# Kernel optimization log

Hardware: AMD Instinct MI355X
Metric: run time of the kernel (lower is better)

The kernel has to match this reference:

```python
import jax, jax.numpy as jnp
import numpy as np

BINS = np.array([1, 2, 3, 4, 8, 16, 32, 64], dtype=np.int32)


def setup_inputs() -> dict:
    N, G, F, H, K = 1024, 620, 20, 150, 128
    D_in = 3 * G + F  # 1880
    key = jax.random.key(0)
    ks = jax.random.split(key, 10)
    g = jax.random.normal(ks[0], (N, G), dtype=jnp.float32)
    si = jax.random.normal(ks[1], (N,), dtype=jnp.float32)
    i1 = jnp.sort(jax.random.randint(ks[2], (N,), 0, 8192)).astype(jnp.int32)
    i2 = jnp.sort(jax.random.randint(ks[3], (N,), 0, 8192)).astype(jnp.int32)
    dist_emb = jax.random.normal(ks[4], (9, F), dtype=jnp.float32) * 0.02
    W1 = jax.random.normal(ks[5], (D_in, H), dtype=jnp.float32) * (1.0 / np.sqrt(D_in))
    b1 = jnp.zeros((H,), jnp.float32)
    W2 = jax.random.normal(ks[6], (H, H), dtype=jnp.float32) * (1.0 / np.sqrt(H))
    b2 = jnp.zeros((H,), jnp.float32)
    W3 = jax.random.normal(ks[7], (H, 1), dtype=jnp.float32) * (1.0 / np.sqrt(H))
    b3 = jnp.zeros((1,), jnp.float32)
    return {"g": g, "si": si, "i1": i1, "i2": i2, "dist_emb": dist_emb,
            "W1": W1, "b1": b1, "W2": W2, "b2": b2, "W3": W3, "b3": b3, "K": K}


def reference(g, si, i1, i2, dist_emb, W1, b1, W2, b2, W3, b3, K):
    # Dropout is inference-disabled; epsilon dummy antecedent appended as last column.
    N, G = g.shape
    # span n's antecedents are spans [max(0, n-K), n); lay out as [N, K] window
    j_idx = jnp.arange(N)[:, None] - K + jnp.arange(K)[None, :]  # [N, K]
    valid = j_idx >= 0
    j = jnp.clip(j_idx, 0, N - 1)
    g_j = g[j]                      # [N, K, G] ragged gather (masked dense)
    g_i = g[:, None, :]             # [N, 1, G]
    # distance feature: bin(i.i2 - j.i1) with idx = #bins <= d
    d = i2[:, None] - i1[j]         # [N, K]
    bin_idx = jnp.searchsorted(jnp.asarray(BINS), d, side='right')
    de = dist_emb[bin_idx]          # [N, K, F]
    pairs = jnp.concatenate(
        [jnp.broadcast_to(g_i, (N, K, G)), g_j, g_i * g_j, de], axis=-1)  # [N, K, 3G+F]
    h = jax.nn.relu(jnp.einsum('nkd,dh->nkh', pairs, W1) + b1)
    h = jax.nn.relu(jnp.einsum('nkh,hm->nkm', h, W2) + b2)
    s = (jnp.einsum('nkh,ho->nko', h, W3) + b3)[..., 0]  # [N, K]
    sij = si[:, None] + si[j] + s
    sij = jnp.where(valid, sij, 0.0)
    eps = jnp.zeros((N, 1), sij.dtype)  # epsilon dummy score
    return jnp.concatenate([sij, eps], axis=-1)  # [N, K+1]
```

## Files before the change

### kernel.cpp

```cpp
#include <hip/hip_runtime.h>
#include <hip/hip_bf16.h>
#include <stdint.h>

typedef __attribute__((ext_vector_type(8))) short short8;
typedef __attribute__((ext_vector_type(4))) float float4_t;

#define N_PTS 1024
#define G_DIM 620
#define G_PAD 640
#define F_DIM 20
#define H_DIM 150
#define H_PAD 160
#define K_WIN 128
#define OUT_C (K_WIN + 1)

__device__ __forceinline__ float bf2f(short u) {
  union { unsigned int i; float f; } x;
  x.i = ((unsigned int)(unsigned short)u) << 16;
  return x.f;
}
__device__ __forceinline__ short f2bf(float f) {
  union { float f; unsigned int i; } x; x.f = f;
  unsigned int u = x.i;
  u += 0x7FFFu + ((u >> 16) & 1u);
  return (short)(u >> 16);
}
__device__ __forceinline__ short f2bf_hw(float f) {
  __hip_bfloat16 h = __float2bfloat16(f);
  union { __hip_bfloat16 h; short s; } u; u.h = h;
  return u.s;
}
__device__ __forceinline__ void gload_lds16(const void* g, void* l) {
  __builtin_amdgcn_global_load_lds(
      (const __attribute__((address_space(1))) unsigned int*)g,
      (__attribute__((address_space(3))) unsigned int*)l, 16, 0, 0);
}

__global__ void prep_pack(const float* __restrict__ g, const float* __restrict__ W1,
                          const float* __restrict__ W2, const float* __restrict__ dist_emb,
                          short* __restrict__ g_bf, short* __restrict__ W1cT,
                          short* __restrict__ W1abT, short* __restrict__ W2T,
                          float* __restrict__ deW) {
  __shared__ float lds[32 * 165];
  const int bx = blockIdx.x, tid = threadIdx.x;
  if (bx < 256) {
    const int n0 = bx * 4;
    for (int c = tid; c < 320; c += 256) {
      int r = c / 80, cc = c - r * 80;
      int n = n0 + r, d0 = cc * 8;
      short8 o;
      if (d0 + 8 <= G_DIM) {
        const float* src = g + n * G_DIM + d0;
        #pragma unroll
        for (int e = 0; e < 8; ++e) o[e] = f2bf(src[e]);
      } else {
        #pragma unroll
        for (int e = 0; e < 8; ++e) {
          int d = d0 + e;
          o[e] = (d < G_DIM) ? f2bf(g[n * G_DIM + d]) : (short)0;
        }
      }
      *(short8*)(g_bf + n * G_PAD + d0) = o;
    }
  } else if (bx < 316) {
    const int tb = bx - 256;
    const int third = tb / 20, dt = tb - third * 20;
    const int d0 = dt * 32;
    for (int c = tid; c < 1280; c += 256) {
      int dr = c / 40, ch4 = c - dr * 40;
      int dd = d0 + dr;
      int w1r = third * G_DIM + dd;
      #pragma unroll
      for (int e = 0; e < 4; ++e) {
        int h = ch4 * 4 + e;
        lds[dr * 165 + h] = (dd < G_DIM && h < H_DIM) ? W1[w1r * H_DIM + h] : 0.f;
      }
    }
    __syncthreads();
    short* outp = (third == 2) ? W1cT : (W1abT + third * H_PAD * G_PAD);
    for (int c = tid; c < 640; c += 256) {
      int h = c >> 2, ch = c & 3;
      short8 o;
      #pragma unroll
      for (int e = 0; e < 8; ++e) o[e] = f2bf(lds[(ch * 8 + e) * 165 + h]);
      *(short8*)(outp + h * G_PAD + d0 + ch * 8) = o;
    }
  } else if (bx < 320) {
    const int base = (bx - 316) * 6400;
    for (int c = tid; c < 6400; c += 256) {
      int q = base + c;
      int m = q / H_PAD, k = q - m * H_PAD;
      W2T[q] = (m < H_DIM && k < H_DIM) ? f2bf(W2[k * H_DIM + m]) : (short)0;
    }
  } else {
    for (int c = tid; c < 9 * H_PAD; c += 256) {
      int b = c / H_PAD, h = c - b * H_PAD;
      float acc = 0.f;
      if (h < H_DIM)
        for (int f = 0; f < F_DIM; ++f)
          acc += dist_emb[b * F_DIM + f] * W1[(3 * G_DIM + f) * H_DIM + h];
      deW[c] = acc;
    }
  }
}

__global__ __launch_bounds__(256) void prep_uv_mfma(
    const short* __restrict__ g_bf, const short* __restrict__ W1abT,
    const short* __restrict__ W1cT, const float* __restrict__ b1,
    float* __restrict__ U, float* __restrict__ V, short* __restrict__ W1cF) {
  if (blockIdx.x >= 32) {
    const int s = (blockIdx.x - 32) + 5 * blockIdx.y;
    const int tid = threadIdx.x;
    #pragma unroll
    for (int it = 0; it < 5; ++it) {
      int slot = tid + 256 * it;
      int lc = slot >> 6, lane = slot & 63;
      int ks = lc / 10, wn = (lc / 5) & 1, nt = lc % 5;
      int lo4 = lane & 15, hi2 = lane >> 4;
      short8 v = *(const short8*)(W1cT + (wn * 80 + nt * 16 + lo4) * G_PAD +
                                  s * 64 + ks * 32 + hi2 * 8);
      *(short8*)(W1cF + (s * 20 + lc) * 512 + lane * 8) = v;
    }
    return;
  }
  __shared__ __align__(16) char sA[32 * 128];
  __shared__ __align__(16) char sB[160 * 128];
  const int m0 = blockIdx.x * 32;
  const int yb = blockIdx.y * H_PAD;
  const int tid = threadIdx.x, lane = tid & 63, wid = tid >> 6;
  const int wm = wid >> 1, wn = wid & 1;
  const int lo4 = lane & 15, hi2 = lane >> 4;
  const int l8 = lane >> 3, c8 = lane & 7;
  const int xe = (c8 ^ (l8 & 7)) * 8;

  const float4_t fz = {0.f, 0.f, 0.f, 0.f};
  float4_t acc[5];
  #pragma unroll
  for (int b = 0; b < 5; ++b) acc[b] = fz;

  for (int step = 0; step < 10; ++step) {
    const int d0 = step * 64;
    {
      int row = wid * 8 + l8;
      gload_lds16(g_bf + (m0 + row) * G_PAD + d0 + xe, sA + (wid * 8) * 128);
    }
    #pragma unroll
    for (int cc = 0; cc < 5; ++cc) {
      int row = wid * 8 + cc * 32 + l8;
      gload_lds16(W1abT + (yb + row) * G_PAD + d0 + xe, sB + (wid * 8 + cc * 32) * 128);
    }
    __syncthreads();
    #pragma unroll
    for (int ks = 0; ks < 2; ++ks) {
      const int kb = ks * 64 + 16 * hi2;
      short8 af, bq[5];
      {
        int row = wm * 16 + lo4;
        af = *((const short8*)(sA + row * 128 + (kb ^ ((row & 7) << 4))));
      }
      #pragma unroll
      for (int nt = 0; nt < 5; ++nt) {
        int row = wn * 80 + nt * 16 + lo4;
        bq[nt] = *((const short8*)(sB + row * 128 + (kb ^ ((row & 7) << 4))));
      }
      #pragma unroll
      for (int nt = 0; nt < 5; ++nt)
        acc[nt] = __builtin_amdgcn_mfma_f32_16x16x32_bf16(af, bq[nt], acc[nt], 0, 0, 0);
    }
    __syncthreads();
  }

  const bool isU = (blockIdx.y == 0);
  float* O = isU ? U : V;
  #pragma unroll
  for (int r = 0; r < 4; ++r) {
    int m = m0 + wm * 16 + hi2 * 4 + r;
    #pragma unroll
    for (int nt = 0; nt < 5; ++nt) {
      int h = wn * 80 + nt * 16 + lo4;
      float v = acc[nt][r];
      if (h < H_DIM) { if (isU) v += b1[h]; } else { v = 0.f; }
      O[m * H_PAD + h] = v;
    }
  }
}

__global__ __launch_bounds__(256, 2) void pair_main(
    const short* __restrict__ g_bf, const short* __restrict__ W1cF,
    const short* __restrict__ W2T, const float* __restrict__ U,
    const float* __restrict__ V, const float* __restrict__ deW,
    const float* __restrict__ si, const int* __restrict__ i1,
    const int* __restrict__ i2, const float* __restrict__ W3,
    const float* __restrict__ b2, const float* __restrict__ b3,
    float* __restrict__ out) {
  __shared__ __align__(16) char smem[49152];
  __shared__ __align__(16) short gi_s[G_PAD];
  __shared__ float sj_s[K_WIN];
  __shared__ unsigned char bin_su[K_WIN];
  __shared__ float s_buf[2][K_WIN];

  char* const P0 = smem;
  char* const P1 = smem + 16384;
  char* const Hb = smem;

  const int bid = blockIdx.x;
  const int i = ((bid & 7) << 7) | (bid >> 3);
  const int tid = threadIdx.x;
  const int lane = tid & 63;
  const int wid = tid >> 6;
  const int wm = wid >> 1, wn = wid & 1;
  const int lo4 = lane & 15, hi2 = lane >> 4;
  const int tc8 = tid & 7;

  if (tid < G_PAD / 8)
    ((short8*)gi_s)[tid] = ((const short8*)(g_bf + i * G_PAD))[tid];
  if (tid < K_WIN) {
    int jr = i - K_WIN + tid, jc = jr < 0 ? 0 : jr;
    int d = i2[i] - i1[jc];
    bin_su[tid] = (unsigned char)((d >= 1) + (d >= 2) + (d >= 3) + (d >= 4) +
                                  (d >= 8) + (d >= 16) + (d >= 32) + (d >= 64));
    sj_s[tid] = si[jc];
  }
  __syncthreads();

  const short8* const bfp = (const short8*)W1cF;

  auto loadBq = [&](int s, short8 (&bq)[2][5]) {
    #pragma unroll
    for (int ks = 0; ks < 2; ++ks)
      #pragma unroll
      for (int nt = 0; nt < 5; ++nt)
        bq[ks][nt] = bfp[(s * 20 + (ks * 2 + wn) * 5 + nt) * 64 + lane];
  };
  auto loadA = [&](int s, short8 (&gjv)[4], short8& gvv) {
    const int d0 = s * 64;
    gvv = *((const short8*)(gi_s + d0 + tc8 * 8));
    #pragma unroll
    for (int cc = 0; cc < 4; ++cc) {
      int c = tid + 256 * cc, row = c >> 3;
      int jr = i - K_WIN + row, jc = jr < 0 ? 0 : jr;
      gjv[cc] = *((const short8*)(g_bf + jc * G_PAD + d0 + tc8 * 8));
    }
  };
  auto writeP = [&](char* P, const short8 (&gjv)[4], const short8& gvv) {
    #pragma unroll
    for (int cc = 0; cc < 4; ++cc) {
      int c = tid + 256 * cc, row = c >> 3;
      short8 p;
      #pragma unroll
      for (int e = 0; e < 8; ++e) p[e] = f2bf_hw(bf2f(gjv[cc][e]) * bf2f(gvv[e]));
      int byte = row * 128 + ((tc8 * 16) ^ ((row & 7) << 4));
      *((short8*)(P + byte)) = p;
    }
  };

  const float4_t fz = {0.f, 0.f, 0.f, 0.f};
  float4_t acc[4][5];
  #pragma unroll
  for (int a = 0; a < 4; ++a)
    #pragma unroll
    for (int b = 0; b < 5; ++b) acc[a][b] = fz;

  auto mfma_step = [&](const char* Pc, const short8 (&bq)[2][5]) {
    __builtin_amdgcn_s_setprio(1);
    #pragma unroll
    for (int ks = 0; ks < 2; ++ks) {
      const int kb = ks * 64 + 16 * hi2;
      short8 af[4];
      #pragma unroll
      for (int mt = 0; mt < 4; ++mt) {
        int row = wm * 64 + mt * 16 + lo4;
        af[mt] = *((const short8*)(Pc + row * 128 + (kb ^ ((row & 7) << 4))));
      }
      #pragma unroll
      for (int mt = 0; mt < 4; ++mt)
        #pragma unroll
        for (int nt = 0; nt < 5; ++nt)
          acc[mt][nt] = __builtin_amdgcn_mfma_f32_16x16x32_bf16(af[mt], bq[ks][nt], acc[mt][nt], 0, 0, 0);
    }
    __builtin_amdgcn_s_setprio(0);
  };

  short8 gjv[4], gvv;
  short8 bqE[2][5], bqO[2][5];
  loadA(0, gjv, gvv);
  loadBq(0, bqE);
  writeP(P0, gjv, gvv);

  #pragma unroll
  for (int ss = 0; ss < 5; ++ss) {
    const int s0 = 2 * ss;
    __syncthreads();
    loadA(s0 + 1, gjv, gvv);
    loadBq(s0 + 1, bqO);
    mfma_step(P0, bqE);
    writeP(P1, gjv, gvv);
    __syncthreads();
    if (ss < 4) {
      loadA(s0 + 2, gjv, gvv);
      loadBq(s0 + 2, bqE);
      mfma_step(P1, bqO);
      writeP(P0, gjv, gvv);
    } else {
      mfma_step(P1, bqO);
    }
  }
  __syncthreads();

  float uih[5];
  #pragma unroll
  for (int nt = 0; nt < 5; ++nt) uih[nt] = U[i * H_PAD + wn * 80 + nt * 16 + lo4];
  #pragma unroll
  for (int mt = 0; mt < 4; ++mt) {
    #pragma unroll
    for (int r = 0; r < 4; ++r) {
      int m = wm * 64 + mt * 16 + hi2 * 4 + r;
      int jr = i - K_WIN + m, jc = jr < 0 ? 0 : jr;
      const float* Vj = V + jc * H_PAD;
      const float* De = deW + bin_su[m] * H_PAD;
      #pragma unroll
      for (int nt = 0; nt < 5; ++nt) {
        int h = wn * 80 + nt * 16 + lo4;
        float val = acc[mt][nt][r] + uih[nt] + Vj[h] + De[h];
        val = (h < H_DIM) ? fmaxf(val, 0.f) : 0.f;
        int tile = h >> 6, hc = h & 63;
        int byte = tile * 16384 + m * 128 + ((hc * 2) ^ ((m & 7) << 4));
        *((short*)(Hb + byte)) = f2bf_hw(val);
      }
    }
  }
  {
    short8 z = {0, 0, 0, 0, 0, 0, 0, 0};
    for (int c = tid; c < 512; c += 256) {
      int row = c >> 2, cb = c & 3;
      int byte = 2 * 16384 + row * 128 + ((64 + cb * 16) ^ ((row & 7) << 4));
      *((short8*)(Hb + byte)) = z;
    }
  }
  __syncthreads();

  float4_t acc2[4][5];
  #pragma unroll
  for (int a = 0; a < 4; ++a)
    #pragma unroll
    for (int b = 0; b < 5; ++b) acc2[a][b] = fz;

  short8 bql[2][5];
  #pragma unroll
  for (int nt = 0; nt < 5; ++nt) {
    int row = wn * 80 + nt * 16 + lo4;
    bql[0][nt] = *(const short8*)(W2T + row * H_PAD + hi2 * 8);
  }
  #pragma unroll
  for (int ks = 0; ks < 5; ++ks) {
    const int cur = ks & 1;
    if (ks < 4) {
      #pragma unroll
      for (int nt = 0; nt < 5; ++nt) {
        int row = wn * 80 + nt * 16 + lo4;
        bql[cur ^ 1][nt] = *(const short8*)(W2T + row * H_PAD + (ks + 1) * 32 + hi2 * 8);
      }
    }
    short8 af[4];
    #pragma unroll
    for (int mt = 0; mt < 4; ++mt) {
      int row = wm * 64 + mt * 16 + lo4;
      int kb = (ks & 1) * 64 + hi2 * 16;
      af[mt] = *((const short8*)(Hb + (ks >> 1) * 16384 + row * 128 + (kb ^ ((row & 7) << 4))));
    }
    __builtin_amdgcn_s_setprio(1);
    #pragma unroll
    for (int mt = 0; mt < 4; ++mt)
      #pragma unroll
      for (int nt = 0; nt < 5; ++nt)
        acc2[mt][nt] = __builtin_amdgcn_mfma_f32_16x16x32_bf16(af[mt], bql[cur][nt], acc2[mt][nt], 0, 0, 0);
    __builtin_amdgcn_s_setprio(0);
  }

  float sp[4][4];
  #pragma unroll
  for (int mt = 0; mt < 4; ++mt)
    #pragma unroll
    for (int r = 0; r < 4; ++r) sp[mt][r] = 0.f;

  #pragma unroll
  for (int nt = 0; nt < 5; ++nt) {
    int h = wn * 80 + nt * 16 + lo4;
    float w3 = (h < H_DIM) ? W3[h] : 0.f;
    float bb = (h < H_DIM) ? b2[h] : 0.f;
    #pragma unroll
    for (int mt = 0; mt < 4; ++mt)
      #pragma unroll
      for (int r = 0; r < 4; ++r) {
        float hv = fmaxf(acc2[mt][nt][r] + bb, 0.f);
        sp[mt][r] += hv * w3;
      }
  }
  #pragma unroll
  for (int mt = 0; mt < 4; ++mt)
    #pragma unroll
    for (int r = 0; r < 4; ++r) {
      float v = sp[mt][r];
      v += __shfl_xor(v, 1);
      v += __shfl_xor(v, 2);
      v += __shfl_xor(v, 4);
      v += __shfl_xor(v, 8);
      sp[mt][r] = v;
    }
  if (lo4 == 0) {
    #pragma unroll
    for (int mt = 0; mt < 4; ++mt)
      #pragma unroll
      for (int r = 0; r < 4; ++r) {
        int m = wm * 64 + mt * 16 + hi2 * 4 + r;
        s_buf[wn][m] = sp[mt][r];
      }
  }
  __syncthreads();

  if (tid < K_WIN) {
    int m = tid;
    int jr = i - K_WIN + m;
    float sij = si[i] + sj_s[m] + s_buf[0][m] + s_buf[1][m] + b3[0];
    out[i * OUT_C + m] = (jr >= 0) ? sij : 0.f;
  }
  if (tid == K_WIN) out[i * OUT_C + K_WIN] = 0.f;
}

extern "C" void kernel_launch(void* const* d_in, const int* in_sizes, int n_in,
                              void* d_out, int out_size, void* d_ws, size_t ws_size,
                              hipStream_t stream) {
  const float* g  = (const float*)d_in[0];
  const float* si = (const float*)d_in[1];
  const int*   i1 = (const int*)d_in[2];
  const int*   i2 = (const int*)d_in[3];
  const float* de = (const float*)d_in[4];
  const float* W1 = (const float*)d_in[5];
  const float* b1 = (const float*)d_in[6];
  const float* W2 = (const float*)d_in[7];
  const float* b2 = (const float*)d_in[8];
  const float* W3 = (const float*)d_in[9];
  const float* b3 = (const float*)d_in[10];
  float* out = (float*)d_out;

  char* ws = (char*)d_ws;
  short* g_bf  = (short*)(ws);
  short* W1cT  = (short*)(ws + 1310720);
  short* W1abT = (short*)(ws + 1515520);
  short* W2T   = (short*)(ws + 1925120);
  float* U     = (float*)(ws + 1976320);
  float* V     = (float*)(ws + 2631680);
  float* deW   = (float*)(ws + 3287040);
  short* W1cF  = (short*)(ws + 3292800);

  prep_pack<<<321, 256, 0, stream>>>(g, W1, W2, de, g_bf, W1cT, W1abT, W2T, deW);
  prep_uv_mfma<<<dim3(37, 2), 256, 0, stream>>>(g_bf, W1abT, W1cT, b1, U, V, W1cF);
  pair_main<<<N_PTS, 256, 0, stream>>>(g_bf, W1cF, W2T, U, V, deW,
                                       si, i1, i2, W3, b2, b3, out);
}
```

Baseline: 72.35 us.

## Stage g_j window via direct global-to-LDS loads and fuse gi product into fragments

Stops loading g_j into registers, multiplying by g_i and writing the product to LDS. Instead the raw g_j window is copied straight from global memory into swizzled LDS with async global-to-LDS loads, and the g_i*g_j product is formed per fragment right before the MFMAs. This frees registers and removes a register round-trip and VALU work from the staging path. Occupancy is also raised by setting launch bounds to 3 blocks per CU. The cost is that both column-half waves now compute the same products, and the tighter register budget may cause spills.

```diff
diff --git a/kernel.cpp b/kernel.cpp
--- a/kernel.cpp
+++ b/kernel.cpp
@@ -185,7 +185,7 @@
   }
 }
 
-__global__ __launch_bounds__(256, 2) void pair_main(
+__global__ __launch_bounds__(256, 3) void pair_main(
     const short* __restrict__ g_bf, const short* __restrict__ W1cF,
     const short* __restrict__ W2T, const float* __restrict__ U,
     const float* __restrict__ V, const float* __restrict__ deW,
@@ -199,8 +199,8 @@
   __shared__ unsigned char bin_su[K_WIN];
   __shared__ float s_buf[2][K_WIN];
 
-  char* const P0 = smem;
-  char* const P1 = smem + 16384;
+  char* const Wn0 = smem;
+  char* const Wn1 = smem + 16384;
   char* const Hb = smem;
 
   const int bid = blockIdx.x;
@@ -210,7 +210,8 @@
   const int wid = tid >> 6;
   const int wm = wid >> 1, wn = wid & 1;
   const int lo4 = lane & 15, hi2 = lane >> 4;
-  const int tc8 = tid & 7;
+  const int l8 = lane >> 3, c8 = lane & 7;
+  const int xe = (c8 ^ (l8 & 7)) * 8;
 
   if (tid < G_PAD / 8)
     ((short8*)gi_s)[tid] = ((const short8*)(g_bf + i * G_PAD))[tid];
@@ -232,25 +233,13 @@
       for (int nt = 0; nt < 5; ++nt)
         bq[ks][nt] = bfp[(s * 20 + (ks * 2 + wn) * 5 + nt) * 64 + lane];
   };
-  auto loadA = [&](int s, short8 (&gjv)[4], short8& gvv) {
+  auto stageWin = [&](int s, char* W) {
     const int d0 = s * 64;
-    gvv = *((const short8*)(gi_s + d0 + tc8 * 8));
     #pragma unroll
     for (int cc = 0; cc < 4; ++cc) {
-      int c = tid + 256 * cc, row = c >> 3;
+      int row = wid * 8 + cc * 32 + l8;
       int jr = i - K_WIN + row, jc = jr < 0 ? 0 : jr;
-      gjv[cc] = *((const short8*)(g_bf + jc * G_PAD + d0 + tc8 * 8));
-    }
-  };
-  auto writeP = [&](char* P, const short8 (&gjv)[4], const short8& gvv) {
-    #pragma unroll
-    for (int cc = 0; cc < 4; ++cc) {
-      int c = tid + 256 * cc, row = c >> 3;
-      short8 p;
-      #pragma unroll
-      for (int e = 0; e < 8; ++e) p[e] = f2bf_hw(bf2f(gjv[cc][e]) * bf2f(gvv[e]));
-      int byte = row * 128 + ((tc8 * 16) ^ ((row & 7) << 4));
-      *((short8*)(P + byte)) = p;
+      gload_lds16(g_bf + jc * G_PAD + d0 + xe, W + (wid * 8 + cc * 32) * 128);
     }
   };
 
@@ -261,49 +250,49 @@
     #pragma unroll
     for (int b = 0; b < 5; ++b) acc[a][b] = fz;
 
-  auto mfma_step = [&](const char* Pc, const short8 (&bq)[2][5]) {
-    __builtin_amdgcn_s_setprio(1);
+  auto mfma_step = [&](int s, const char* Wc, const short8 (&bq)[2][5]) {
     #pragma unroll
     for (int ks = 0; ks < 2; ++ks) {
+      short8 giv = *(const short8*)(gi_s + s * 64 + ks * 32 + hi2 * 8);
+      float gf[8];
+      #pragma unroll
+      for (int e = 0; e < 8; ++e) gf[e] = bf2f(giv[e]);
       const int kb = ks * 64 + 16 * hi2;
       short8 af[4];
       #pragma unroll
       for (int mt = 0; mt < 4; ++mt) {
         int row = wm * 64 + mt * 16 + lo4;
-        af[mt] = *((const short8*)(Pc + row * 128 + (kb ^ ((row & 7) << 4))));
-      }
+        short8 gj = *((const short8*)(Wc + row * 128 + (kb ^ ((row & 7) << 4))));
+        #pragma unroll
+        for (int e = 0; e < 8; ++e) af[mt][e] = f2bf_hw(bf2f(gj[e]) * gf[e]);
+      }
+      __builtin_amdgcn_s_setprio(1);
       #pragma unroll
       for (int mt = 0; mt < 4; ++mt)
         #pragma unroll
         for (int nt = 0; nt < 5; ++nt)
           acc[mt][nt] = __builtin_amdgcn_mfma_f32_16x16x32_bf16(af[mt], bq[ks][nt], acc[mt][nt], 0, 0, 0);
-    }
-    __builtin_amdgcn_s_setprio(0);
+      __builtin_amdgcn_s_setprio(0);
+    }
   };
 
-  short8 gjv[4], gvv;
   short8 bqE[2][5], bqO[2][5];
-  loadA(0, gjv, gvv);
+  stageWin(0, Wn0);
   loadBq(0, bqE);
-  writeP(P0, gjv, gvv);
 
   #pragma unroll
   for (int ss = 0; ss < 5; ++ss) {
     const int s0 = 2 * ss;
     __syncthreads();
-    loadA(s0 + 1, gjv, gvv);
+    stageWin(s0 + 1, Wn1);
     loadBq(s0 + 1, bqO);
-    mfma_step(P0, bqE);
-    writeP(P1, gjv, gvv);
+    mfma_step(s0, Wn0, bqE);
     __syncthreads();
     if (ss < 4) {
-      loadA(s0 + 2, gjv, gvv);
+      stageWin(s0 + 2, Wn0);
       loadBq(s0 + 2, bqE);
-      mfma_step(P1, bqO);
-      writeP(P0, gjv, gvv);
-    } else {
-      mfma_step(P1, bqO);
-    }
+    }
+    mfma_step(s0 + 1, Wn1, bqO);
   }
   __syncthreads();
 
```

After: 143.5 us. +98.3%, slower.
